# Optimization experiments

Measured on AMD Instinct MI355X. Metric: run time of the kernel, lower is better.

## Reference

```python
import jax, jax.numpy as jnp
import numpy as np

HEADS = 4
C = 128            # per-head out channels (hard-coded 128 in the module)
NEG_SLOPE_ATT = 0.2   # GATConv attention leaky_relu slope
NEG_SLOPE = 0.01      # F.leaky_relu default slope


def _diag_output_ids(num_groups, n):
    # ids = base_i + n*j + j for group i, agent j; base_i = i * n^2
    i = np.arange(num_groups)[:, None] * (n * n)
    j = np.arange(n)[None, :] * (n + 1)
    return jnp.asarray((i + j).reshape(-1))


def setup_inputs() -> dict:
    key = jax.random.key(0)
    ks = jax.random.split(key, 12)
    num_groups, n_agents = 12, 48
    N = num_groups * n_agents * n_agents      # 27648 nodes
    E = 442368
    F_in, edge_dim, hidden = 256, 16, 256
    s = 0.05
    return {
        "x": jax.random.normal(ks[0], (N, F_in), jnp.float32),
        "edge_index": jax.random.randint(ks[1], (2, E), 0, N, jnp.int32),
        "edge_attr": jax.random.normal(ks[2], (E, edge_dim), jnp.float32),
        "num_groups": num_groups,
        "agents_per_group": n_agents,
        "W": jax.random.normal(ks[3], (F_in, HEADS * C), jnp.float32) * s,
        "att_src": jax.random.normal(ks[4], (HEADS, C), jnp.float32) * s,
        "att_dst": jax.random.normal(ks[5], (HEADS, C), jnp.float32) * s,
        "W_edge": jax.random.normal(ks[6], (edge_dim, HEADS * C), jnp.float32) * s,
        "att_edge": jax.random.normal(ks[7], (HEADS, C), jnp.float32) * s,
        "bias_gat": jnp.zeros((HEADS * C,), jnp.float32),
        "fc_W": jax.random.normal(ks[8], (HEADS * C, hidden), jnp.float32) * s,
        "fc_b": jnp.zeros((hidden,), jnp.float32),
    }


def _gat_conv(x, src, dst, edge_attr_full, W, att_src, att_dst, W_edge, att_edge, bias):
    N = x.shape[0]
    h = (x @ W).reshape(N, HEADS, C)                       # [N,H,C]
    a_src = jnp.einsum('nhc,hc->nh', h, att_src)           # [N,H]
    a_dst = jnp.einsum('nhc,hc->nh', h, att_dst)
    he = (edge_attr_full @ W_edge).reshape(-1, HEADS, C)   # [E',H,C]
    a_edge = jnp.einsum('ehc,hc->eh', he, att_edge)
    logits = jax.nn.leaky_relu(a_src[src] + a_dst[dst] + a_edge, NEG_SLOPE_ATT)
    # segment softmax over incoming edges of each dst node
    m = jax.ops.segment_max(logits, dst, num_segments=N)   # [N,H]
    e = jnp.exp(logits - m[dst])
    s = jax.ops.segment_sum(e, dst, num_segments=N)
    alpha = e / (s[dst] + 1e-16)                           # [E',H]
    msg = h[src] * alpha[..., None]                        # [E',H,C]
    out = jax.ops.segment_sum(msg, dst, num_segments=N)    # [N,H,C]
    return out.reshape(N, HEADS * C) + bias


def reference(x, edge_index, edge_attr, num_groups, agents_per_group,
              W, att_src, att_dst, W_edge, att_edge, bias_gat, fc_W, fc_b):
    N = x.shape[0]
    # add self-loops (PyG default), self-loop edge_attr = mean fill
    loops = jnp.arange(N, dtype=edge_index.dtype)
    src = jnp.concatenate([edge_index[0], loops])
    dst = jnp.concatenate([edge_index[1], loops])
    ea = jnp.concatenate([edge_attr,
                          jnp.broadcast_to(edge_attr.mean(0), (N, edge_attr.shape[1]))])
    h = jax.nn.leaky_relu(
        _gat_conv(x, src, dst, ea, W, att_src, att_dst, W_edge, att_edge, bias_gat),
        NEG_SLOPE)
    ids = _diag_output_ids(num_groups, agents_per_group)
    # fc_output + leaky_relu then diagonal index-select (select first: same math)
    return jax.nn.leaky_relu(h[ids] @ fc_W + fc_b, NEG_SLOPE)
```

## Files before the change

kernel.cpp:

```cpp
#include <hip/hip_runtime.h>

#define NNODES 27648
#define NEDGES 442368
#define FIN    256
#define HC     512
#define NH     4
#define CDIM   128
#define NAG    48
#define NGRP   12
#define N2     2304
#define NOUT   576
#define CAP    128
#define EDIM   16
#define MPART  512

__device__ __forceinline__ float lrelu(float v, float s){ return v > 0.0f ? v : s * v; }

__device__ __forceinline__ float wsum(float v){
  #pragma unroll
  for (int off = 32; off; off >>= 1) v += __shfl_xor(v, off, 64);
  return v;
}
__device__ __forceinline__ float wmax(float v){
  #pragma unroll
  for (int off = 32; off; off >>= 1) v = fmaxf(v, __shfl_xor(v, off, 64));
  return v;
}

__global__ __launch_bounds__(256) void k_pre(
    const float* __restrict__ W, const float* __restrict__ att_src,
    const float* __restrict__ att_dst, const float* __restrict__ W_edge,
    const float* __restrict__ att_edge, const float* __restrict__ ea,
    float* __restrict__ ws_, float* __restrict__ wd_, float* __restrict__ we_,
    int* __restrict__ counts, float4* __restrict__ easum_part){
  int b = blockIdx.x;
  int tid = threadIdx.x;
  if (b < 11) {
    int g = b * 256 + tid;
    if (g < 1024) {
      int f = g >> 2, h = g & 3;
      const float4* wp = (const float4*)(W + f*HC + h*CDIM);
      const float4* ap = (const float4*)(att_src + h*CDIM);
      float s = 0.f;
      #pragma unroll 8
      for (int c4 = 0; c4 < CDIM/4; c4++){
        float4 wv = wp[c4], av = ap[c4];
        s += wv.x*av.x + wv.y*av.y + wv.z*av.z + wv.w*av.w;
      }
      ws_[g] = s;
    } else if (g < 2048) {
      int gg = g - 1024; int f = gg >> 2, h = gg & 3;
      const float4* wp = (const float4*)(W + f*HC + h*CDIM);
      const float4* ap = (const float4*)(att_dst + h*CDIM);
      float s = 0.f;
      #pragma unroll 8
      for (int c4 = 0; c4 < CDIM/4; c4++){
        float4 wv = wp[c4], av = ap[c4];
        s += wv.x*av.x + wv.y*av.y + wv.z*av.z + wv.w*av.w;
      }
      wd_[gg] = s;
    } else if (g < 2112) {
      int gg = g - 2048; int d = gg >> 2, h = gg & 3;
      const float4* wp = (const float4*)(W_edge + d*HC + h*CDIM);
      const float4* ap = (const float4*)(att_edge + h*CDIM);
      float s = 0.f;
      #pragma unroll 8
      for (int c4 = 0; c4 < CDIM/4; c4++){
        float4 wv = wp[c4], av = ap[c4];
        s += wv.x*av.x + wv.y*av.y + wv.z*av.z + wv.w*av.w;
      }
      we_[gg] = s;
    } else if (g < 2112 + NOUT) {
      counts[g - 2112] = 0;
    }
  } else {
    int pb = b - 11;
    const float4* p = (const float4*)ea;
    const int total = NEDGES * 4;
    float4 acc = make_float4(0.f, 0.f, 0.f, 0.f);
    for (int i = pb*256 + tid; i < total; i += MPART*256){
      float4 v = p[i];
      acc.x += v.x; acc.y += v.y; acc.z += v.z; acc.w += v.w;
    }
    #pragma unroll
    for (int off = 4; off <= 32; off <<= 1){
      acc.x += __shfl_xor(acc.x, off, 64);
      acc.y += __shfl_xor(acc.y, off, 64);
      acc.z += __shfl_xor(acc.z, off, 64);
      acc.w += __shfl_xor(acc.w, off, 64);
    }
    __shared__ float4 sd4[16];
    int lane = tid & 63, wave = tid >> 6;
    if (lane < 4) sd4[wave*4 + lane] = acc;
    __syncthreads();
    if (tid < 4){
      float4 t = sd4[tid];
      float4 a = sd4[4+tid], c = sd4[8+tid], d = sd4[12+tid];
      t.x += a.x + c.x + d.x; t.y += a.y + c.y + d.y;
      t.z += a.z + c.z + d.z; t.w += a.w + c.w + d.w;
      easum_part[pb*4 + tid] = t;
    }
  }
}

__global__ __launch_bounds__(256) void k_scan(const int* __restrict__ ei,
    const float* __restrict__ ea, const float* __restrict__ we_,
    int* __restrict__ counts, int* __restrict__ slist, float* __restrict__ aed,
    const float* __restrict__ easum_part, float* __restrict__ easum){
  int tid = threadIdx.x;
  if (blockIdx.x == NEDGES/256){
    int col = tid & 15, part = tid >> 4;
    float s = 0.f;
    for (int pb = 0; pb < MPART/16; pb++)
      s += easum_part[(part*(MPART/16) + pb)*16 + col];
    __shared__ float sd[256];
    sd[tid] = s;
    __syncthreads();
    if (tid < 16){
      float t = 0.f;
      #pragma unroll
      for (int i = 0; i < 16; i++) t += sd[i*16 + tid];
      easum[tid] = t;
    }
    return;
  }
  int e = blockIdx.x*256 + tid;
  int dst = ei[NEDGES + e];
  int r = dst % N2;
  if (r % 49) return;
  int row = (dst / N2) * NAG + r / 49;
  int pos = atomicAdd(&counts[row], 1);
  if (pos >= CAP) return;
  slist[row*CAP + pos] = ei[e];
  const float* eap = ea + (size_t)e*EDIM;
  float a0=0.f,a1=0.f,a2=0.f,a3=0.f;
  #pragma unroll
  for (int d = 0; d < EDIM; d++){
    float v = eap[d];
    a0 += v*we_[d*4+0]; a1 += v*we_[d*4+1]; a2 += v*we_[d*4+2]; a3 += v*we_[d*4+3];
  }
  float* ap = aed + (size_t)(row*CAP+pos)*4;
  ap[0]=a0; ap[1]=a1; ap[2]=a2; ap[3]=a3;
}

__global__ __launch_bounds__(256) void k_mega(const float* __restrict__ x,
    const float* __restrict__ ws_, const float* __restrict__ wd_,
    const float* __restrict__ we_, const float* __restrict__ easum,
    const int* __restrict__ counts, const int* __restrict__ slist,
    const float* __restrict__ aed,
    const float* __restrict__ W, const float* __restrict__ bias,
    const float* __restrict__ fcW, const float* __restrict__ fcb,
    float* __restrict__ out){
  __shared__ float lg[(CAP+1)*4];
  __shared__ int   srcs[CAP];
  __shared__ float adst_s[4];
  __shared__ float zs[4*256];
  __shared__ float hs[512];
  int row = blockIdx.x;
  int g = row / NAG, j = row - g*NAG;
  int dst = g*N2 + j*49;
  int tid = threadIdx.x;
  int lane = tid & 63, wave = tid >> 6;
  int k = counts[row]; if (k > CAP) k = CAP;

  float wsr[4][4];
  #pragma unroll
  for (int q = 0; q < 4; q++){
    float4 t = *(const float4*)(ws_ + (lane*4+q)*4);
    wsr[q][0]=t.x; wsr[q][1]=t.y; wsr[q][2]=t.z; wsr[q][3]=t.w;
  }

  for (int i = wave; i < k; i += 4){
    int src = slist[row*CAP + i];
    float4 aedv = *(const float4*)(aed + (size_t)(row*CAP+i)*4);
    float4 xv = *(const float4*)(x + (size_t)src*FIN + lane*4);
    float p0 = xv.x*wsr[0][0] + xv.y*wsr[1][0] + xv.z*wsr[2][0] + xv.w*wsr[3][0];
    float p1 = xv.x*wsr[0][1] + xv.y*wsr[1][1] + xv.z*wsr[2][1] + xv.w*wsr[3][1];
    float p2 = xv.x*wsr[0][2] + xv.y*wsr[1][2] + xv.z*wsr[2][2] + xv.w*wsr[3][2];
    float p3 = xv.x*wsr[0][3] + xv.y*wsr[1][3] + xv.z*wsr[2][3] + xv.w*wsr[3][3];
    p0 = wsum(p0); p1 = wsum(p1); p2 = wsum(p2); p3 = wsum(p3);
    if (lane == 0){
      srcs[i] = src;
      lg[i*4+0] = p0 + aedv.x; lg[i*4+1] = p1 + aedv.y;
      lg[i*4+2] = p2 + aedv.z; lg[i*4+3] = p3 + aedv.w;
    }
  }

  if (wave == 0){
    float wdr[4][4];
    #pragma unroll
    for (int q = 0; q < 4; q++){
      float4 t = *(const float4*)(wd_ + (lane*4+q)*4);
      wdr[q][0]=t.x; wdr[q][1]=t.y; wdr[q][2]=t.z; wdr[q][3]=t.w;
    }
    float4 xv = *(const float4*)(x + (size_t)dst*FIN + lane*4);
    float pd[4], ps[4];
    #pragma unroll
    for (int h = 0; h < 4; h++){
      pd[h] = xv.x*wdr[0][h] + xv.y*wdr[1][h] + xv.z*wdr[2][h] + xv.w*wdr[3][h];
      ps[h] = xv.x*wsr[0][h] + xv.y*wsr[1][h] + xv.z*wsr[2][h] + xv.w*wsr[3][h];
    }
    const float invE = 1.0f/(float)NEDGES;
    float md = (lane < 16) ? easum[lane]*invE : 0.f;
    float al[4];
    #pragma unroll
    for (int h = 0; h < 4; h++){
      float c = (lane < 16) ? md*we_[lane*4+h] : 0.f;
      al[h] = wsum(c);
      pd[h] = wsum(pd[h]);
      ps[h] = wsum(ps[h]);
    }
    if (lane == 0){
      #pragma unroll
      for (int h = 0; h < 4; h++){
        adst_s[h] = pd[h];
        lg[k*4+h] = ps[h] + al[h];
      }
    }
  }
  __syncthreads();

  {
    int h = wave;
    float ad = adst_s[h];
    float m = -1e30f;
    for (int i = lane; i <= k; i += 64){
      float v = lrelu(lg[i*4+h] + ad, 0.2f);
      lg[i*4+h] = v;
      m = fmaxf(m, v);
    }
    m = wmax(m);
    float s = 0.f;
    for (int i = lane; i <= k; i += 64){
      float e = __expf(lg[i*4+h] - m);
      lg[i*4+h] = e;
      s += e;
    }
    s = wsum(s);
    float inv = 1.0f/(s + 1e-16f);
    for (int i = lane; i <= k; i += 64) lg[i*4+h] *= inv;
  }
  __syncthreads();

  {
    int f = tid;
    float a0=0.f,a1=0.f,a2=0.f,a3=0.f;
    for (int i = 0; i < k; i++){
      float xv = x[(size_t)srcs[i]*FIN + f];
      a0 += lg[i*4+0]*xv; a1 += lg[i*4+1]*xv; a2 += lg[i*4+2]*xv; a3 += lg[i*4+3]*xv;
    }
    {
      float xv = x[(size_t)dst*FIN + f];
      a0 += lg[k*4+0]*xv; a1 += lg[k*4+1]*xv; a2 += lg[k*4+2]*xv; a3 += lg[k*4+3]*xv;
    }
    zs[0*256+f]=a0; zs[1*256+f]=a1; zs[2*256+f]=a2; zs[3*256+f]=a3;
  }
  __syncthreads();

  {
    int o1 = tid, o2 = tid + 256;
    const float* z1 = zs + ((tid >> 7) << 8);
    const float* z2 = zs + 512 + ((tid >> 7) << 8);
    const float* W1 = W + o1;
    float acc1 = 0.f, acc2 = 0.f;
    for (int ff = 0; ff < 256; ff += 8){
      #pragma unroll
      for (int u = 0; u < 8; u++){
        float w1 = W1[(size_t)(ff+u)*HC];
        float w2 = W1[(size_t)(ff+u)*HC + 256];
        acc1 += z1[ff+u]*w1;
        acc2 += z2[ff+u]*w2;
      }
    }
    hs[o1] = lrelu(acc1 + bias[o1], 0.01f);
    hs[o2] = lrelu(acc2 + bias[o2], 0.01f);
  }
  __syncthreads();

  {
    const float* Fw = fcW + tid;
    float acc = 0.f;
    for (int k0 = 0; k0 < 512; k0 += 8){
      #pragma unroll
      for (int u = 0; u < 8; u++)
        acc += hs[k0+u] * Fw[(size_t)(k0+u)*256];
    }
    out[(size_t)row*256 + tid] = lrelu(acc + fcb[tid], 0.01f);
  }
}

extern "C" void kernel_launch(void* const* d_in, const int* in_sizes, int n_in,
                              void* d_out, int out_size, void* d_ws, size_t ws_size,
                              hipStream_t stream) {
  const float* x        = (const float*)d_in[0];
  const int*   ei       = (const int*)  d_in[1];
  const float* ea       = (const float*)d_in[2];
  const float* W        = (const float*)d_in[5];
  const float* att_src  = (const float*)d_in[6];
  const float* att_dst  = (const float*)d_in[7];
  const float* W_edge   = (const float*)d_in[8];
  const float* att_edge = (const float*)d_in[9];
  const float* bias     = (const float*)d_in[10];
  const float* fcW      = (const float*)d_in[11];
  const float* fcb      = (const float*)d_in[12];
  float* out = (float*)d_out;

  float* w = (float*)d_ws;
  float*  ws_       = w;
  float*  wd_       = w + 1024;
  float*  we_       = w + 2048;
  float*  easum     = w + 2112;
  int*    counts    = (int*)(w + 2128);
  float*  easum_p   = w + 2704;
  int*    slist     = (int*)(w + 10896);
  float*  aed       = w + 84624;

  k_pre<<<11 + MPART, 256, 0, stream>>>(W, att_src, att_dst, W_edge, att_edge, ea,
                                        ws_, wd_, we_, counts, (float4*)easum_p);
  k_scan<<<NEDGES/256 + 1, 256, 0, stream>>>(ei, ea, we_, counts, slist, aed,
                                             easum_p, easum);
  k_mega<<<NOUT, 256, 0, stream>>>(x, ws_, wd_, we_, easum, counts, slist, aed,
                                   W, bias, fcW, fcb, out);
}
```

Baseline: 161.0 us.

## Restructure mega kernel aggregation and GEMVs with float4 loads and split-K partials

The edge aggregation now has each wave handle a strided subset of edges with float4 row loads, keeping per-head accumulators in registers. The four per-wave partials are then reduced through shared memory. Both dense matvecs (W projection and fc) switch to float4 column loads with a split-K layout and a shared-memory reduction. The goal is fewer, wider global loads and more memory-level parallelism per block, at the cost of about 30KB of extra shared memory, which can reduce occupancy.

After: 156.6 us. 1.03x faster.

```diff
diff --git a/kernel.cpp b/kernel.cpp
--- a/kernel.cpp
+++ b/kernel.cpp
@@ -13,6 +13,7 @@
 #define CAP    128
 #define EDIM   16
 #define MPART  512
+
 
 __device__ __forceinline__ float lrelu(float v, float s){ return v > 0.0f ? v : s * v; }
 
@@ -151,11 +152,14 @@
     const float* __restrict__ W, const float* __restrict__ bias,
     const float* __restrict__ fcW, const float* __restrict__ fcb,
     float* __restrict__ out){
-  __shared__ float lg[(CAP+1)*4];
-  __shared__ int   srcs[CAP];
-  __shared__ float adst_s[4];
-  __shared__ float zs[4*256];
-  __shared__ float hs[512];
+  __shared__ float  lg[(CAP+1)*4];
+  __shared__ int    srcs[CAP+1];
+  __shared__ float  adst_s[4];
+  __shared__ float4 pz4[4*256];
+  __shared__ float4 zs4[256];
+  __shared__ float4 ph4[256];
+  __shared__ float  hs[512];
+  __shared__ float4 pq4[256];
   int row = blockIdx.x;
   int g = row / NAG, j = row - g*NAG;
   int dst = g*N2 + j*49;
@@ -216,6 +220,7 @@
         adst_s[h] = pd[h];
         lg[k*4+h] = ps[h] + al[h];
       }
+      srcs[k] = dst;
     }
   }
   __syncthreads();
@@ -243,49 +248,85 @@
   __syncthreads();
 
   {
-    int f = tid;
-    float a0=0.f,a1=0.f,a2=0.f,a3=0.f;
-    for (int i = 0; i < k; i++){
-      float xv = x[(size_t)srcs[i]*FIN + f];
-      a0 += lg[i*4+0]*xv; a1 += lg[i*4+1]*xv; a2 += lg[i*4+2]*xv; a3 += lg[i*4+3]*xv;
-    }
-    {
-      float xv = x[(size_t)dst*FIN + f];
-      a0 += lg[k*4+0]*xv; a1 += lg[k*4+1]*xv; a2 += lg[k*4+2]*xv; a3 += lg[k*4+3]*xv;
-    }
-    zs[0*256+f]=a0; zs[1*256+f]=a1; zs[2*256+f]=a2; zs[3*256+f]=a3;
-  }
-  __syncthreads();
-
-  {
-    int o1 = tid, o2 = tid + 256;
-    const float* z1 = zs + ((tid >> 7) << 8);
-    const float* z2 = zs + 512 + ((tid >> 7) << 8);
-    const float* W1 = W + o1;
-    float acc1 = 0.f, acc2 = 0.f;
-    for (int ff = 0; ff < 256; ff += 8){
+    float acc[4][4];
+    #pragma unroll
+    for (int h = 0; h < 4; h++)
       #pragma unroll
-      for (int u = 0; u < 8; u++){
-        float w1 = W1[(size_t)(ff+u)*HC];
-        float w2 = W1[(size_t)(ff+u)*HC + 256];
-        acc1 += z1[ff+u]*w1;
-        acc2 += z2[ff+u]*w2;
-      }
-    }
-    hs[o1] = lrelu(acc1 + bias[o1], 0.01f);
-    hs[o2] = lrelu(acc2 + bias[o2], 0.01f);
-  }
-  __syncthreads();
-
-  {
-    const float* Fw = fcW + tid;
-    float acc = 0.f;
-    for (int k0 = 0; k0 < 512; k0 += 8){
-      #pragma unroll
-      for (int u = 0; u < 8; u++)
-        acc += hs[k0+u] * Fw[(size_t)(k0+u)*256];
-    }
-    out[(size_t)row*256 + tid] = lrelu(acc + fcb[tid], 0.01f);
+      for (int c = 0; c < 4; c++) acc[h][c] = 0.f;
+    for (int i = wave; i <= k; i += 4){
+      int src = srcs[i];
+      float4 xv = *(const float4*)(x + (size_t)src*FIN + lane*4);
+      float a0 = lg[i*4+0], a1 = lg[i*4+1], a2 = lg[i*4+2], a3 = lg[i*4+3];
+      acc[0][0] += a0*xv.x; acc[0][1] += a0*xv.y; acc[0][2] += a0*xv.z; acc[0][3] += a0*xv.w;
+      acc[1][0] += a1*xv.x; acc[1][1] += a1*xv.y; acc[1][2] += a1*xv.z; acc[1][3] += a1*xv.w;
+      acc[2][0] += a2*xv.x; acc[2][1] += a2*xv.y; acc[2][2] += a2*xv.z; acc[2][3] += a2*xv.w;
+      acc[3][0] += a3*xv.x; acc[3][1] += a3*xv.y; acc[3][2] += a3*xv.z; acc[3][3] += a3*xv.w;
+    }
+    #pragma unroll
+    for (int h = 0; h < 4; h++)
+      pz4[wave*256 + h*64 + lane] =
+        make_float4(acc[h][0], acc[h][1], acc[h][2], acc[h][3]);
+  }
+  __syncthreads();
+  {
+    float4 a = pz4[0*256+tid], b = pz4[1*256+tid],
+           c = pz4[2*256+tid], d = pz4[3*256+tid];
+    zs4[tid] = make_float4(a.x+b.x+c.x+d.x, a.y+b.y+c.y+d.y,
+                           a.z+b.z+c.z+d.z, a.w+b.w+c.w+d.w);
+  }
+  __syncthreads();
+
+  {
+    int cg = tid & 127;
+    int half = tid >> 7;
+    int h = cg >> 5;
+    const float* zp = (const float*)zs4 + h*256 + half*128;
+    const float4* Wp = (const float4*)(W + (size_t)half*128*HC) + cg;
+    float4 acc = make_float4(0.f,0.f,0.f,0.f);
+    #pragma unroll 8
+    for (int r = 0; r < 128; r++){
+      float4 w4 = Wp[(size_t)r*(HC/4)];
+      float zv = zp[r];
+      acc.x += zv*w4.x; acc.y += zv*w4.y; acc.z += zv*w4.z; acc.w += zv*w4.w;
+    }
+    ph4[half*128 + cg] = acc;
+  }
+  __syncthreads();
+  if (tid < 128){
+    float4 a = ph4[tid], b = ph4[128+tid];
+    float4 bs = *(const float4*)(bias + 4*tid);
+    hs[4*tid+0] = lrelu(a.x+b.x+bs.x, 0.01f);
+    hs[4*tid+1] = lrelu(a.y+b.y+bs.y, 0.01f);
+    hs[4*tid+2] = lrelu(a.z+b.z+bs.z, 0.01f);
+    hs[4*tid+3] = lrelu(a.w+b.w+bs.w, 0.01f);
+  }
+  __syncthreads();
+
+  {
+    int cg = tid & 63;
+    int q  = tid >> 6;
+    const float4* Fp = (const float4*)(fcW + (size_t)q*128*256) + cg;
+    const float* hp = hs + q*128;
+    float4 acc = make_float4(0.f,0.f,0.f,0.f);
+    #pragma unroll 8
+    for (int r = 0; r < 128; r++){
+      float4 w4 = Fp[(size_t)r*64];
+      float hv = hp[r];
+      acc.x += hv*w4.x; acc.y += hv*w4.y; acc.z += hv*w4.z; acc.w += hv*w4.w;
+    }
+    pq4[q*64 + cg] = acc;
+  }
+  __syncthreads();
+  if (tid < 64){
+    float4 a = pq4[tid],      b = pq4[64+tid];
+    float4 c = pq4[128+tid],  d = pq4[192+tid];
+    float4 bs = *(const float4*)(fcb + 4*tid);
+    float4 o;
+    o.x = lrelu(a.x+b.x+c.x+d.x+bs.x, 0.01f);
+    o.y = lrelu(a.y+b.y+c.y+d.y+bs.y, 0.01f);
+    o.z = lrelu(a.z+b.z+c.z+d.z+bs.z, 0.01f);
+    o.w = lrelu(a.w+b.w+c.w+d.w+bs.w, 0.01f);
+    *(float4*)(out + (size_t)row*256 + 4*tid) = o;
   }
 }
 
```
